# Kernel tuning notes

Measured on AMD Instinct MI355X. Metric: run time of the kernel, lower is better.

The kernel has to match this reference:

```python
import jax, jax.numpy as jnp
import numpy as np

# Dims: B batch, C=P channels (features per pixel), H*W=N pixels, M ELM models, Q=1 hidden units
M, Q, B, C, H, W_SP = 4, 1, 32, 1024, 28, 28
P = C
N = H * W_SP
EPS = 1e-10


def _lcg_weights(m, n, seed):
    """Deterministic LCG pseudo-random weights, z-score standardized (ELM_AE init)."""
    L = m * n
    a, b, c = L + 2, L + 3, float(L) ** 2
    v = np.zeros(L, dtype=np.float64)
    v[0] = seed + 1.0
    for i in range(1, L):
        v[i] = (a * v[i - 1] + b) % c
    v = (v - v.mean()) / (v.std() + EPS)
    return v.reshape(m, n).astype(np.float32)


def setup_inputs() -> dict:
    key = jax.random.key(0)
    x = jax.random.normal(key, (B, C, H, W_SP), dtype=jnp.float32)
    # One Q x P random input-weight matrix per ELM model, seed = model * (Q * P)
    Wm = jnp.stack([jnp.asarray(_lcg_weights(Q, P, model * (Q * P))) for model in range(M)])  # [M, Q, P]
    return {"x": x, "Wm": Wm}


def reference(x, Wm):
    b, c, h, w = x.shape
    # _norm('l2', ...): per-channel L2 normalization over (h, w), as F.normalize(dim=(1,2))
    norms = jnp.linalg.norm(x.reshape(b, c, h * w), axis=-1)[:, :, None, None]  # [B, C, 1, 1]
    xn = x / jnp.maximum(norms, EPS)
    X = xn.reshape(b, c, h * w)  # meta activation map per sample: [B, P, N]
    # ELM-AE hidden layer, batched over (sample, model): g = sigmoid(W @ X)
    G = jax.nn.sigmoid(jnp.einsum('mqp,bpn->bmqn', Wm, X))  # [B, M, Q, N]
    # fit_AE: output weights beta = pinv(g^T) @ X^T  -> [Q, P]
    pinvGt = jnp.linalg.pinv(jnp.swapaxes(G, -1, -2))       # [B, M, Q, N]
    beta = jnp.einsum('bmqn,bpn->bmqp', pinvGt, X)          # [B, M, Q, P]
    # sum over the M models; Q == 1 so flatten (Q, P) -> Q*P features
    feats = beta.sum(axis=1).reshape(b, -1)                 # [B, Q*P]
    return jnp.nan_to_num(feats)
```

## Files before the change

kernel.cpp:

```cpp
#include <hip/hip_runtime.h>
#include <math.h>

#define BATCH 32
#define CH    1024
#define NPix  784
#define MMOD  4
#define NPC   16
#define PPC   64
#define T2    832

__device__ __forceinline__ float wave_reduce(float s) {
    #pragma unroll
    for (int off = 32; off; off >>= 1) s += __shfl_down(s, off, 64);
    return s;
}

__global__ __launch_bounds__(T2) void k_norm_z(const float* __restrict__ x,
                                               const float* __restrict__ Wm,
                                               float* __restrict__ inv_norm,
                                               float* __restrict__ zpart) {
    __shared__ float inv_lds[PPC];
    __shared__ float wlds[MMOD][PPC];
    const int blk = blockIdx.x;
    const int b  = blk >> 4;
    const int pc = blk & (NPC - 1);
    const int t = threadIdx.x;
    const int wv = t >> 6, lane = t & 63;
    const float* xb = x + ((size_t)b * CH + (size_t)pc * PPC) * NPix;

    for (int row = wv; row < PPC; row += 13) {
        const float4* r4 = (const float4*)(xb + (size_t)row * NPix);
        float s = 0.f;
        #pragma unroll
        for (int i = 0; i < 3; i++) {
            float4 v = r4[i * 64 + lane];
            s += v.x*v.x + v.y*v.y + v.z*v.z + v.w*v.w;
        }
        if (lane < 4) {
            float4 v = r4[192 + lane];
            s += v.x*v.x + v.y*v.y + v.z*v.z + v.w*v.w;
        }
        s = wave_reduce(s);
        if (lane == 0) {
            float inv = 1.f / fmaxf(sqrtf(s), 1e-10f);
            inv_lds[row] = inv;
            inv_norm[b * CH + pc * PPC + row] = inv;
        }
    }
    __syncthreads();

    if (t < PPC) {
        float inv = inv_lds[t];
        #pragma unroll
        for (int m = 0; m < MMOD; m++)
            wlds[m][t] = Wm[m * CH + pc * PPC + t] * inv;
    }
    __syncthreads();

    if (t < NPix) {
        float a0 = 0.f, a1 = 0.f, a2 = 0.f, a3 = 0.f;
        const float* xp = xb + t;
        #pragma unroll 8
        for (int pp = 0; pp < PPC; pp++) {
            float xv = xp[(size_t)pp * NPix];
            a0 += wlds[0][pp] * xv;
            a1 += wlds[1][pp] * xv;
            a2 += wlds[2][pp] * xv;
            a3 += wlds[3][pp] * xv;
        }
        size_t base = (((size_t)b * NPC + pc) * MMOD) * NPix + t;
        zpart[base]            = a0;
        zpart[base + NPix]     = a1;
        zpart[base + 2 * NPix] = a2;
        zpart[base + 3 * NPix] = a3;
    }
}

__global__ __launch_bounds__(T2) void k_gh(const float* __restrict__ zpart,
                                           float* __restrict__ h) {
    __shared__ float red[13][MMOD];
    __shared__ float s2s[MMOD];
    const int b = blockIdx.x;
    const int t = threadIdx.x;
    const int wv = t >> 6, lane = t & 63;
    const bool act = (t < NPix);

    float g[MMOD];
    #pragma unroll
    for (int m = 0; m < MMOD; m++) {
        float z = 0.f;
        if (act) {
            #pragma unroll
            for (int pc = 0; pc < NPC; pc++)
                z += zpart[(((size_t)b * NPC + pc) * MMOD + m) * NPix + t];
        }
        g[m] = act ? 1.f / (1.f + expf(-z)) : 0.f;
    }
    #pragma unroll
    for (int m = 0; m < MMOD; m++) {
        float s = wave_reduce(g[m] * g[m]);
        if (lane == 0) red[wv][m] = s;
    }
    __syncthreads();
    if (t < MMOD) {
        float s = 0.f;
        #pragma unroll
        for (int w = 0; w < 13; w++) s += red[w][t];
        s2s[t] = fmaxf(s, 1e-30f);
    }
    __syncthreads();
    if (act) {
        float hv = 0.f;
        #pragma unroll
        for (int m = 0; m < MMOD; m++) hv += g[m] / s2s[m];
        h[(size_t)b * NPix + t] = hv;
    }
}

__global__ __launch_bounds__(256) void k_out(const float* __restrict__ x,
                                             const float* __restrict__ h,
                                             const float* __restrict__ inv_norm,
                                             float* __restrict__ out) {
    const int r = blockIdx.x * 4 + (threadIdx.x >> 6);
    const int lane = threadIdx.x & 63;
    const int b = r >> 10;
    const float4* x4 = (const float4*)(x + (size_t)r * NPix);
    const float4* h4 = (const float4*)(h + (size_t)b * NPix);
    float s = 0.f;
    #pragma unroll
    for (int i = 0; i < 3; i++) {
        float4 xv = x4[i * 64 + lane];
        float4 hv = h4[i * 64 + lane];
        s += xv.x*hv.x + xv.y*hv.y + xv.z*hv.z + xv.w*hv.w;
    }
    if (lane < 4) {
        float4 xv = x4[192 + lane];
        float4 hv = h4[192 + lane];
        s += xv.x*hv.x + xv.y*hv.y + xv.z*hv.z + xv.w*hv.w;
    }
    s = wave_reduce(s);
    if (lane == 0) {
        float v = s * inv_norm[r];
        if (!(v == v)) v = 0.f;
        v = fminf(fmaxf(v, -3.402823466e+38f), 3.402823466e+38f);
        out[r] = v;
    }
}

extern "C" void kernel_launch(void* const* d_in, const int* in_sizes, int n_in,
                              void* d_out, int out_size, void* d_ws, size_t ws_size,
                              hipStream_t stream) {
    const float* x  = (const float*)d_in[0];
    const float* Wm = (const float*)d_in[1];
    float* out = (float*)d_out;
    float* wsf = (float*)d_ws;

    float* inv_norm = wsf;
    float* zpart    = inv_norm + BATCH * CH;
    float* h        = zpart + (size_t)BATCH * NPC * MMOD * NPix;

    k_norm_z<<<BATCH * NPC, T2, 0, stream>>>(x, Wm, inv_norm, zpart);
    k_gh<<<BATCH, T2, 0, stream>>>(zpart, h);
    k_out<<<BATCH * CH / 4, 256, 0, stream>>>(x, h, inv_norm, out);
}
```

Baseline: 184.7 us.

## Fuse norm and projection in registers with per-wave row ownership and LDS atomics

Each wave now owns 8 channel rows. It loads each row once into registers, computes the L2 norm from those values, and accumulates the four model projections in registers. This replaces the previous two passes over x (norm pass, then a column-wise projection pass that reread x). Per-wave partials are merged with LDS atomics before being written out. The grid doubles to 32 chunks of 32 channels per batch, which doubles the zpart traffic that k_gh must reduce, and the register-heavy accumulators (52 floats plus 13 loads) may lower occupancy.

```diff
diff --git a/kernel.cpp b/kernel.cpp
--- a/kernel.cpp
+++ b/kernel.cpp
@@ -5,8 +5,9 @@
 #define CH    1024
 #define NPix  784
 #define MMOD  4
-#define NPC   16
-#define PPC   64
+#define NPC   32
+#define PPC   32
+#define K1B   256
 #define T2    832
 
 __device__ __forceinline__ float wave_reduce(float s) {
@@ -15,65 +16,63 @@
     return s;
 }
 
-__global__ __launch_bounds__(T2) void k_norm_z(const float* __restrict__ x,
-                                               const float* __restrict__ Wm,
-                                               float* __restrict__ inv_norm,
-                                               float* __restrict__ zpart) {
-    __shared__ float inv_lds[PPC];
-    __shared__ float wlds[MMOD][PPC];
+__global__ __launch_bounds__(K1B) void k_norm_z(const float* __restrict__ x,
+                                                const float* __restrict__ Wm,
+                                                float* __restrict__ inv_norm,
+                                                float* __restrict__ zpart) {
+    __shared__ float zlds[MMOD * NPix];
     const int blk = blockIdx.x;
-    const int b  = blk >> 4;
+    const int b  = blk >> 5;
     const int pc = blk & (NPC - 1);
     const int t = threadIdx.x;
     const int wv = t >> 6, lane = t & 63;
     const float* xb = x + ((size_t)b * CH + (size_t)pc * PPC) * NPix;
 
-    for (int row = wv; row < PPC; row += 13) {
-        const float4* r4 = (const float4*)(xb + (size_t)row * NPix);
+    for (int i = t; i < MMOD * NPix; i += K1B) zlds[i] = 0.f;
+
+    float zacc[MMOD][13];
+    #pragma unroll
+    for (int m = 0; m < MMOD; m++)
+        #pragma unroll
+        for (int k = 0; k < 13; k++) zacc[m][k] = 0.f;
+
+    __syncthreads();
+
+    #pragma unroll
+    for (int rr = 0; rr < 8; rr++) {
+        const int row = wv * 8 + rr;
+        const int p = pc * PPC + row;
+        const float* xr = xb + (size_t)row * NPix;
+        float xv[13];
+        #pragma unroll
+        for (int k = 0; k < 12; k++) xv[k] = xr[k * 64 + lane];
+        xv[12] = (lane < 16) ? xr[768 + lane] : 0.f;
         float s = 0.f;
         #pragma unroll
-        for (int i = 0; i < 3; i++) {
-            float4 v = r4[i * 64 + lane];
-            s += v.x*v.x + v.y*v.y + v.z*v.z + v.w*v.w;
-        }
-        if (lane < 4) {
-            float4 v = r4[192 + lane];
-            s += v.x*v.x + v.y*v.y + v.z*v.z + v.w*v.w;
-        }
-        s = wave_reduce(s);
-        if (lane == 0) {
-            float inv = 1.f / fmaxf(sqrtf(s), 1e-10f);
-            inv_lds[row] = inv;
-            inv_norm[b * CH + pc * PPC + row] = inv;
+        for (int k = 0; k < 13; k++) s += xv[k] * xv[k];
+        #pragma unroll
+        for (int off = 32; off; off >>= 1) s += __shfl_xor(s, off, 64);
+        const float inv = 1.f / fmaxf(sqrtf(s), 1e-10f);
+        if (lane == 0) inv_norm[b * CH + p] = inv;
+        #pragma unroll
+        for (int m = 0; m < MMOD; m++) {
+            const float w = Wm[m * CH + p] * inv;
+            #pragma unroll
+            for (int k = 0; k < 13; k++) zacc[m][k] += w * xv[k];
         }
     }
+
+    #pragma unroll
+    for (int m = 0; m < MMOD; m++)
+        #pragma unroll
+        for (int k = 0; k < 13; k++) {
+            const int n = k * 64 + lane;
+            if (n < NPix) atomicAdd(&zlds[m * NPix + n], zacc[m][k]);
+        }
     __syncthreads();
 
-    if (t < PPC) {
-        float inv = inv_lds[t];
-        #pragma unroll
-        for (int m = 0; m < MMOD; m++)
-            wlds[m][t] = Wm[m * CH + pc * PPC + t] * inv;
-    }
-    __syncthreads();
-
-    if (t < NPix) {
-        float a0 = 0.f, a1 = 0.f, a2 = 0.f, a3 = 0.f;
-        const float* xp = xb + t;
-        #pragma unroll 8
-        for (int pp = 0; pp < PPC; pp++) {
-            float xv = xp[(size_t)pp * NPix];
-            a0 += wlds[0][pp] * xv;
-            a1 += wlds[1][pp] * xv;
-            a2 += wlds[2][pp] * xv;
-            a3 += wlds[3][pp] * xv;
-        }
-        size_t base = (((size_t)b * NPC + pc) * MMOD) * NPix + t;
-        zpart[base]            = a0;
-        zpart[base + NPix]     = a1;
-        zpart[base + 2 * NPix] = a2;
-        zpart[base + 3 * NPix] = a3;
-    }
+    float* zp = zpart + (size_t)blk * (MMOD * NPix);
+    for (int i = t; i < MMOD * NPix; i += K1B) zp[i] = zlds[i];
 }
 
 __global__ __launch_bounds__(T2) void k_gh(const float* __restrict__ zpart,
@@ -90,7 +89,7 @@
     for (int m = 0; m < MMOD; m++) {
         float z = 0.f;
         if (act) {
-            #pragma unroll
+            #pragma unroll 8
             for (int pc = 0; pc < NPC; pc++)
                 z += zpart[(((size_t)b * NPC + pc) * MMOD + m) * NPix + t];
         }
@@ -159,7 +158,7 @@
     float* zpart    = inv_norm + BATCH * CH;
     float* h        = zpart + (size_t)BATCH * NPC * MMOD * NPix;
 
-    k_norm_z<<<BATCH * NPC, T2, 0, stream>>>(x, Wm, inv_norm, zpart);
+    k_norm_z<<<BATCH * NPC, K1B, 0, stream>>>(x, Wm, inv_norm, zpart);
     k_gh<<<BATCH, T2, 0, stream>>>(zpart, h);
     k_out<<<BATCH * CH / 4, 256, 0, stream>>>(x, h, inv_norm, out);
 }
```

New measurement: 241.0 us. +30.5%, slower.

## Hold channel tile in registers to fuse norm and projection, halve tile size

Applied to the files above, without the earlier changes.

The first kernel now loads each thread's pixel column for 32 channels into registers once and reuses it for both the per-channel squared-norm reduction and the four-model projection. Previously x was read twice within the block, once row-wise for the norm and once column-wise for the projection. Norms are computed with DPP row reductions plus an LDS cross-wave sum, and the scaled weights are packed as float4 in LDS. Halving the channels per block doubles the grid to 1024 blocks but also doubles the zpart partials that k_gh must read and sum. It also raises register pressure from the 32-element array.

```diff
diff --git a/kernel.cpp b/kernel.cpp
--- a/kernel.cpp
+++ b/kernel.cpp
@@ -5,8 +5,8 @@
 #define CH    1024
 #define NPix  784
 #define MMOD  4
-#define NPC   16
-#define PPC   64
+#define NPC   32
+#define PPC   32
 #define T2    832
 
 __device__ __forceinline__ float wave_reduce(float s) {
@@ -15,60 +15,80 @@
     return s;
 }
 
-__global__ __launch_bounds__(T2) void k_norm_z(const float* __restrict__ x,
-                                               const float* __restrict__ Wm,
-                                               float* __restrict__ inv_norm,
-                                               float* __restrict__ zpart) {
-    __shared__ float inv_lds[PPC];
-    __shared__ float wlds[MMOD][PPC];
+__device__ __forceinline__ float dpp_wave_sum(float v) {
+    int x;
+    x = __builtin_amdgcn_update_dpp(0, __builtin_bit_cast(int, v), 0x111, 0xf, 0xf, true);
+    v += __builtin_bit_cast(float, x);
+    x = __builtin_amdgcn_update_dpp(0, __builtin_bit_cast(int, v), 0x112, 0xf, 0xf, true);
+    v += __builtin_bit_cast(float, x);
+    x = __builtin_amdgcn_update_dpp(0, __builtin_bit_cast(int, v), 0x114, 0xf, 0xf, true);
+    v += __builtin_bit_cast(float, x);
+    x = __builtin_amdgcn_update_dpp(0, __builtin_bit_cast(int, v), 0x118, 0xf, 0xf, true);
+    v += __builtin_bit_cast(float, x);
+    x = __builtin_amdgcn_update_dpp(0, __builtin_bit_cast(int, v), 0x142, 0xa, 0xf, true);
+    v += __builtin_bit_cast(float, x);
+    x = __builtin_amdgcn_update_dpp(0, __builtin_bit_cast(int, v), 0x143, 0xc, 0xf, true);
+    v += __builtin_bit_cast(float, x);
+    return v;
+}
+
+__global__ __launch_bounds__(T2) void k_nz(const float* __restrict__ x,
+                                           const float* __restrict__ Wm,
+                                           float* __restrict__ inv_norm,
+                                           float* __restrict__ zpart) {
+    __shared__ float sq_l[PPC * 13];
+    __shared__ float4 wl4[PPC];
     const int blk = blockIdx.x;
-    const int b  = blk >> 4;
+    const int b  = blk >> 5;
     const int pc = blk & (NPC - 1);
     const int t = threadIdx.x;
     const int wv = t >> 6, lane = t & 63;
+    const bool act = (t < NPix);
     const float* xb = x + ((size_t)b * CH + (size_t)pc * PPC) * NPix;
+    const float* xp = xb + (act ? t : 0);
 
-    for (int row = wv; row < PPC; row += 13) {
-        const float4* r4 = (const float4*)(xb + (size_t)row * NPix);
-        float s = 0.f;
+    float xv[PPC];
+    #pragma unroll
+    for (int pp = 0; pp < PPC; pp++) xv[pp] = xp[(size_t)pp * NPix];
+    if (!act) {
         #pragma unroll
-        for (int i = 0; i < 3; i++) {
-            float4 v = r4[i * 64 + lane];
-            s += v.x*v.x + v.y*v.y + v.z*v.z + v.w*v.w;
-        }
-        if (lane < 4) {
-            float4 v = r4[192 + lane];
-            s += v.x*v.x + v.y*v.y + v.z*v.z + v.w*v.w;
-        }
-        s = wave_reduce(s);
-        if (lane == 0) {
-            float inv = 1.f / fmaxf(sqrtf(s), 1e-10f);
-            inv_lds[row] = inv;
-            inv_norm[b * CH + pc * PPC + row] = inv;
-        }
+        for (int pp = 0; pp < PPC; pp++) xv[pp] = 0.f;
+    }
+
+    #pragma unroll
+    for (int pp = 0; pp < PPC; pp++) {
+        float s = dpp_wave_sum(xv[pp] * xv[pp]);
+        if (lane == 63) sq_l[pp * 13 + wv] = s;
     }
     __syncthreads();
 
     if (t < PPC) {
-        float inv = inv_lds[t];
+        float s = 0.f;
         #pragma unroll
-        for (int m = 0; m < MMOD; m++)
-            wlds[m][t] = Wm[m * CH + pc * PPC + t] * inv;
+        for (int w = 0; w < 13; w++) s += sq_l[t * 13 + w];
+        const float inv = 1.f / fmaxf(sqrtf(s), 1e-10f);
+        const int p = pc * PPC + t;
+        inv_norm[b * CH + p] = inv;
+        float4 w4;
+        w4.x = Wm[0 * CH + p] * inv;
+        w4.y = Wm[1 * CH + p] * inv;
+        w4.z = Wm[2 * CH + p] * inv;
+        w4.w = Wm[3 * CH + p] * inv;
+        wl4[t] = w4;
     }
     __syncthreads();
 
-    if (t < NPix) {
+    if (act) {
         float a0 = 0.f, a1 = 0.f, a2 = 0.f, a3 = 0.f;
-        const float* xp = xb + t;
-        #pragma unroll 8
+        #pragma unroll
         for (int pp = 0; pp < PPC; pp++) {
-            float xv = xp[(size_t)pp * NPix];
-            a0 += wlds[0][pp] * xv;
-            a1 += wlds[1][pp] * xv;
-            a2 += wlds[2][pp] * xv;
-            a3 += wlds[3][pp] * xv;
+            float4 w = wl4[pp];
+            a0 += w.x * xv[pp];
+            a1 += w.y * xv[pp];
+            a2 += w.z * xv[pp];
+            a3 += w.w * xv[pp];
         }
-        size_t base = (((size_t)b * NPC + pc) * MMOD) * NPix + t;
+        size_t base = ((size_t)blk * MMOD) * NPix + t;
         zpart[base]            = a0;
         zpart[base + NPix]     = a1;
         zpart[base + 2 * NPix] = a2;
@@ -90,7 +110,7 @@
     for (int m = 0; m < MMOD; m++) {
         float z = 0.f;
         if (act) {
-            #pragma unroll
+            #pragma unroll 8
             for (int pc = 0; pc < NPC; pc++)
                 z += zpart[(((size_t)b * NPC + pc) * MMOD + m) * NPix + t];
         }
@@ -159,7 +179,7 @@
     float* zpart    = inv_norm + BATCH * CH;
     float* h        = zpart + (size_t)BATCH * NPC * MMOD * NPix;
 
-    k_norm_z<<<BATCH * NPC, T2, 0, stream>>>(x, Wm, inv_norm, zpart);
+    k_nz<<<BATCH * NPC, T2, 0, stream>>>(x, Wm, inv_norm, zpart);
     k_gh<<<BATCH, T2, 0, stream>>>(zpart, h);
     k_out<<<BATCH * CH / 4, 256, 0, stream>>>(x, h, inv_norm, out);
 }
```

Measured after the change: 182.5 us. No clear change (-1.2%).
